# Kernel optimization log

Hardware: AMD Instinct MI355X
Metric: run time of the kernel (lower is better)

Reference implementation:

```python
import jax, jax.numpy as jnp
import numpy as np
import math

D_MODEL = 128
N_HEADS = 4
DIM_FF = 256
B, L = 4, 2048
EPS = 1e-5
NEG = -1e9


def _layernorm(x, g, b):
    mu = jnp.mean(x, axis=-1, keepdims=True)
    var = jnp.mean((x - mu) ** 2, axis=-1, keepdims=True)
    return (x - mu) * jax.lax.rsqrt(var + EPS) * g + b


def setup_inputs() -> dict:
    key = jax.random.key(0)
    ks = jax.random.split(key, 16)
    s = 1.0 / math.sqrt(D_MODEL)
    return {
        "h": jax.random.normal(ks[0], (B, L, D_MODEL), jnp.float32),
        "attn_bias": jax.random.normal(ks[1], (B, N_HEADS, L, L), jnp.float32),
        "node_mask": jax.random.randint(ks[2], (B, L), 0, 2).astype(jnp.float32),
        "sparse_mask": jax.random.randint(ks[3], (B, L, L), 0, 2).astype(bool),
        "w_qkv": jax.random.normal(ks[4], (3 * D_MODEL, D_MODEL), jnp.float32) * s,
        "b_qkv": jnp.zeros((3 * D_MODEL,), jnp.float32),
        "w_out": jax.random.normal(ks[5], (D_MODEL, D_MODEL), jnp.float32) * s,
        "b_out": jnp.zeros((D_MODEL,), jnp.float32),
        "w_ff1": jax.random.normal(ks[6], (DIM_FF, D_MODEL), jnp.float32) * s,
        "b_ff1": jnp.zeros((DIM_FF,), jnp.float32),
        "w_ff2": jax.random.normal(ks[7], (D_MODEL, DIM_FF), jnp.float32) * (1.0 / math.sqrt(DIM_FF)),
        "b_ff2": jnp.zeros((D_MODEL,), jnp.float32),
        "ln1_g": jnp.ones((D_MODEL,), jnp.float32),
        "ln1_b": jnp.zeros((D_MODEL,), jnp.float32),
        "ln2_g": jnp.ones((D_MODEL,), jnp.float32),
        "ln2_b": jnp.zeros((D_MODEL,), jnp.float32),
    }


def reference(h, attn_bias, node_mask, sparse_mask, w_qkv, b_qkv, w_out, b_out,
              w_ff1, b_ff1, w_ff2, b_ff2, ln1_g, ln1_b, ln2_g, ln2_b):
    bsz, lsz, dsz = h.shape
    dk = dsz // N_HEADS
    qkv = h @ w_qkv.T + b_qkv  # [B,L,3D]
    q, k, v = jnp.split(qkv, 3, axis=-1)
    # [B,L,D] -> [B,H,L,dk]
    q = q.reshape(bsz, lsz, N_HEADS, dk).transpose(0, 2, 1, 3)
    k = k.reshape(bsz, lsz, N_HEADS, dk).transpose(0, 2, 1, 3)
    v = v.reshape(bsz, lsz, N_HEADS, dk).transpose(0, 2, 1, 3)
    scores = jnp.einsum("bhqd,bhkd->bhqk", q, k) / math.sqrt(dk)
    scores = scores + attn_bias
    scores = jnp.where(sparse_mask[:, None, :, :], scores, NEG)
    key_mask = node_mask[:, None, None, :] > 0
    scores = jnp.where(key_mask, scores, NEG)
    attn = jax.nn.softmax(scores, axis=-1)
    attn = attn * (node_mask[:, None, :, None] > 0).astype(attn.dtype)
    out = jnp.einsum("bhqk,bhkd->bhqd", attn, v)
    out = out.transpose(0, 2, 1, 3).reshape(bsz, lsz, dsz)
    out = out @ w_out.T + b_out
    h1 = _layernorm(h + out, ln1_g, ln1_b)
    ff = jax.nn.relu(h1 @ w_ff1.T + b_ff1) @ w_ff2.T + b_ff2
    h2 = _layernorm(h1 + ff, ln2_g, ln2_b)
    return h2 * node_mask[:, :, None]
```

## Files before the change

kernel.cpp:

```cpp
#include <hip/hip_runtime.h>
#include <math.h>

#define NEG_INF (-1e9f)
#define EPS 1e-5f

typedef __attribute__((ext_vector_type(8))) short short8;
typedef __attribute__((ext_vector_type(4))) float floatx4;

__device__ __forceinline__ unsigned short f2bf(float x) {
    union { float f; unsigned u; } v; v.f = x;
    unsigned r = v.u + 0x7fffu + ((v.u >> 16) & 1u);
    return (unsigned short)(r >> 16);
}

__device__ __forceinline__ void gl2lds16(const void* g, void* l) {
    __builtin_amdgcn_global_load_lds(
        (const __attribute__((address_space(1))) unsigned int*)g,
        (__attribute__((address_space(3))) unsigned int*)l, 16, 0, 0);
}

__global__ void prep_kernel(const unsigned int* __restrict__ sm, int* __restrict__ flag,
                            const float* __restrict__ nm, unsigned int* __restrict__ nmb) {
    if (blockIdx.x == 0) {
        __shared__ int bad;
        if (threadIdx.x == 0) bad = 0;
        __syncthreads();
        for (int i = threadIdx.x; i < 4096; i += 256) {
            if (sm[i] > 1u) bad = 1;
        }
        __syncthreads();
        if (threadIdx.x == 0) *flag = bad;
    } else {
        const int t = threadIdx.x;
        const int b = t >> 6, w32 = t & 63;
        unsigned u = 0;
#pragma unroll
        for (int j = 0; j < 32; ++j)
            u |= (nm[b * 2048 + w32 * 32 + j] > 0.f ? 1u : 0u) << j;
        nmb[t] = u;
    }
}

__global__ void mask_prep_kernel(const unsigned char* __restrict__ smraw,
                                 const int* __restrict__ flag,
                                 const unsigned int* __restrict__ nmb,
                                 unsigned int* __restrict__ cbits) {
    const int idx = blockIdx.x * 256 + threadIdx.x;
    const int b = idx >> 17;
    const int q = (idx >> 6) & 2047;
    const int w32 = idx & 63;
    unsigned u = 0;
    if (*flag) {
        const uint4* p = reinterpret_cast<const uint4*>(
            smraw + (size_t)(b * 2048 + q) * 2048 + w32 * 32);
        uint4 a = p[0], c = p[1];
        unsigned wd0 = a.x, wd1 = a.y, wd2 = a.z, wd3 = a.w;
        unsigned wd4 = c.x, wd5 = c.y, wd6 = c.z, wd7 = c.w;
#define BYTES4(v, sh) \
        u |= ((v) & 0xffu ? 1u : 0u) << (sh); \
        u |= ((v) & 0xff00u ? 1u : 0u) << ((sh) + 1); \
        u |= ((v) & 0xff0000u ? 1u : 0u) << ((sh) + 2); \
        u |= ((v) & 0xff000000u ? 1u : 0u) << ((sh) + 3);
        BYTES4(wd0, 0) BYTES4(wd1, 4) BYTES4(wd2, 8) BYTES4(wd3, 12)
        BYTES4(wd4, 16) BYTES4(wd5, 20) BYTES4(wd6, 24) BYTES4(wd7, 28)
#undef BYTES4
    } else {
        const uint4* p = reinterpret_cast<const uint4*>(
            reinterpret_cast<const unsigned int*>(smraw) + (size_t)(b * 2048 + q) * 2048 + w32 * 32);
#pragma unroll
        for (int wi = 0; wi < 8; ++wi) {
            uint4 a = p[wi];
            u |= (a.x ? 1u : 0u) << (wi * 4);
            u |= (a.y ? 1u : 0u) << (wi * 4 + 1);
            u |= (a.z ? 1u : 0u) << (wi * 4 + 2);
            u |= (a.w ? 1u : 0u) << (wi * 4 + 3);
        }
    }
    cbits[idx] = u & nmb[b * 64 + w32];
}

__global__ void transpose_all_kernel(const float* __restrict__ w_qkv, const float* __restrict__ w_out,
                                     const float* __restrict__ w_ff1, const float* __restrict__ w_ff2,
                                     float* __restrict__ wqkvT, float* __restrict__ woutT,
                                     float* __restrict__ wff1T, float* __restrict__ wff2T) {
    int idx = blockIdx.x * 256 + threadIdx.x;
    if (idx < 49152) {
        int r = idx / 128, c = idx % 128;
        wqkvT[c * 384 + r] = w_qkv[idx];
    } else if (idx < 65536) {
        int i = idx - 49152; int r = i / 128, c = i % 128;
        woutT[c * 128 + r] = w_out[i];
    } else if (idx < 98304) {
        int i = idx - 65536; int r = i / 128, c = i % 128;
        wff1T[c * 256 + r] = w_ff1[i];
    } else {
        int i = idx - 98304; int r = i / 256, c = i % 256;
        wff2T[c * 128 + r] = w_ff2[i];
    }
}

__global__ void qkv_kernel(const float* __restrict__ h, const float* __restrict__ wT,
                           const float* __restrict__ bqkv,
                           unsigned short* __restrict__ qb, unsigned short* __restrict__ kbm,
                           unsigned short* __restrict__ vtb) {
    __shared__ __align__(16) float hs[16 * 128];
    const int tid = threadIdx.x;
    const int row0 = blockIdx.x * 16;
    for (int i = tid; i < 2048; i += 384) hs[i] = h[row0 * 128 + i];
    __syncthreads();

    const int c = tid;
    float acc[16];
#pragma unroll
    for (int r = 0; r < 16; ++r) acc[r] = 0.f;

    for (int d0 = 0; d0 < 128; d0 += 4) {
        float w0 = wT[(d0 + 0) * 384 + c];
        float w1 = wT[(d0 + 1) * 384 + c];
        float w2 = wT[(d0 + 2) * 384 + c];
        float w3 = wT[(d0 + 3) * 384 + c];
#pragma unroll
        for (int r = 0; r < 16; ++r) {
            float4 h4 = *reinterpret_cast<const float4*>(&hs[r * 128 + d0]);
            acc[r] = fmaf(w0, h4.x, acc[r]);
            acc[r] = fmaf(w1, h4.y, acc[r]);
            acc[r] = fmaf(w2, h4.z, acc[r]);
            acc[r] = fmaf(w3, h4.w, acc[r]);
        }
    }
    const int part = c >> 7;
    const int cc = c & 127;
    const int head = cc >> 5;
    const int dd = cc & 31;
    const float bias = bqkv[c];
    const float scale = (part == 0) ? 0.17677669529663687f : 1.0f;
#pragma unroll
    for (int r = 0; r < 16; ++r) {
        int grow = row0 + r;
        int b = grow >> 11, l = grow & 2047;
        int bh = b * 4 + head;
        unsigned short val = f2bf((acc[r] + bias) * scale);
        if (part == 0)      qb[((size_t)bh * 2048 + l) * 32 + dd] = val;
        else if (part == 1) kbm[((size_t)bh * 2048 + l) * 32 + dd] = val;
        else                vtb[((size_t)bh * 32 + dd) * 2048 + l] = val;
    }
}

__global__ __launch_bounds__(256, 2) void attn_kernel(
        const unsigned short* __restrict__ qb, const unsigned short* __restrict__ kbm,
        const unsigned short* __restrict__ vtb, const float* __restrict__ bias,
        const unsigned int* __restrict__ cbits, const float* __restrict__ nmask,
        float* __restrict__ aout) {
    __shared__ __align__(16) unsigned short k_lds[2][64 * 32];
    __shared__ __align__(16) unsigned short v_lds[2][32 * 64];
    __shared__ __align__(16) float bias_lds[2][64 * 64];
    __shared__ __align__(16) unsigned short p_lds[4][16 * 72];

    const int tid = threadIdx.x;
    const int w = tid >> 6, L = tid & 63;
    const int lb = (blockIdx.x & 7) * 64 + (blockIdx.x >> 3);
    const int bh = lb >> 5, qt = lb & 31;
    const int b = bh >> 2, hh = bh & 3;
    const int q0b = qt * 64;
    const int q = L & 15, g = L >> 4;

    const unsigned short* kb_g = kbm + (size_t)bh * 2048 * 32;
    const unsigned short* vb_g = vtb + (size_t)bh * 32 * 2048;
    const float* bias_q0 = bias + ((size_t)bh * 2048 + q0b) * 2048;
    const short8 qf = *reinterpret_cast<const short8*>(
        qb + ((size_t)bh * 2048 + q0b + w * 16 + q) * 32 + g * 8);
    const unsigned int* crow = cbits + (size_t)(b * 2048 + q0b + w * 16 + q) * 64;

    const int r_k = tid >> 2;
    const size_t k_src0 = (size_t)r_k * 32 + (((tid & 3) ^ (r_k & 3)) << 3);
    const int d_v = tid >> 3;
    const size_t v_src0 = (size_t)d_v * 2048 + (((tid & 7) ^ (d_v & 7)) << 3);
    const int br = tid >> 4;
    const int bsw = ((tid & 15) ^ br) << 2;

    auto stage = [&](int buf, int kt) {
        const int k0 = kt * 64;
        gl2lds16(kb_g + (size_t)k0 * 32 + k_src0, (char*)(&k_lds[buf][0]) + w * 1024);
        gl2lds16(vb_g + k0 + v_src0, (char*)(&v_lds[buf][0]) + w * 1024);
#pragma unroll
        for (int i = 0; i < 4; ++i)
            gl2lds16(bias_q0 + (size_t)(br + 16 * i) * 2048 + k0 + bsw,
                     (char*)(&bias_lds[buf][0]) + i * 4096 + w * 1024);
    };

    stage(0, 0);
    __syncthreads();

    float mrun = -3.0e38f, lrun = 0.f;
    floatx4 o0 = {0.f, 0.f, 0.f, 0.f}, o1 = {0.f, 0.f, 0.f, 0.f};
    const floatx4 zacc = {0.f, 0.f, 0.f, 0.f};
    unsigned short* pl = &p_lds[w][q * 72];

    const int ksw = (g ^ (q & 3)) << 4;
    const int vsw0 = ((g) ^ (q & 7)) << 4;
    const int vsw1 = ((g + 4) ^ (q & 7)) << 4;
    const int brow = (w * 16 + q) * 256;

    for (int t = 0; t < 32; ++t) {
        const int cur = t & 1;
        if (t + 1 < 32) stage(cur ^ 1, t + 1);

        const char* kl = (const char*)(&k_lds[cur][0]);
        short8 kf0 = *reinterpret_cast<const short8*>(kl + (q     ) * 64 + ksw);
        short8 kf1 = *reinterpret_cast<const short8*>(kl + (16 + q) * 64 + ksw);
        short8 kf2 = *reinterpret_cast<const short8*>(kl + (32 + q) * 64 + ksw);
        short8 kf3 = *reinterpret_cast<const short8*>(kl + (48 + q) * 64 + ksw);
        const char* vl = (const char*)(&v_lds[cur][0]);
        short8 vf00 = *reinterpret_cast<const short8*>(vl + (q     ) * 128 + vsw0);
        short8 vf01 = *reinterpret_cast<const short8*>(vl + (q     ) * 128 + vsw1);
        short8 vf10 = *reinterpret_cast<const short8*>(vl + (16 + q) * 128 + vsw0);
        short8 vf11 = *reinterpret_cast<const short8*>(vl + (16 + q) * 128 + vsw1);
        uint2 cw = *reinterpret_cast<const uint2*>(crow + t * 2);

        float s[16];
        {
            floatx4 r0 = __builtin_amdgcn_mfma_f32_16x16x32_bf16(kf0, qf, zacc, 0, 0, 0);
            floatx4 r1 = __builtin_amdgcn_mfma_f32_16x16x32_bf16(kf1, qf, zacc, 0, 0, 0);
            floatx4 r2 = __builtin_amdgcn_mfma_f32_16x16x32_bf16(kf2, qf, zacc, 0, 0, 0);
            floatx4 r3 = __builtin_amdgcn_mfma_f32_16x16x32_bf16(kf3, qf, zacc, 0, 0, 0);
            s[0] = r0[0]; s[1] = r0[1]; s[2] = r0[2]; s[3] = r0[3];
            s[4] = r1[0]; s[5] = r1[1]; s[6] = r1[2]; s[7] = r1[3];
            s[8] = r2[0]; s[9] = r2[1]; s[10] = r2[2]; s[11] = r2[3];
            s[12] = r3[0]; s[13] = r3[1]; s[14] = r3[2]; s[15] = r3[3];
        }
        const char* bl = (const char*)(&bias_lds[cur][0]);
        float4 bq0 = *reinterpret_cast<const float4*>(bl + brow + (((0 + g) ^ q) << 4));
        float4 bq1 = *reinterpret_cast<const float4*>(bl + brow + (((4 + g) ^ q) << 4));
        float4 bq2 = *reinterpret_cast<const float4*>(bl + brow + (((8 + g) ^ q) << 4));
        float4 bq3 = *reinterpret_cast<const float4*>(bl + brow + (((12 + g) ^ q) << 4));
        float bvv[16];
        bvv[0] = bq0.x; bvv[1] = bq0.y; bvv[2] = bq0.z; bvv[3] = bq0.w;
        bvv[4] = bq1.x; bvv[5] = bq1.y; bvv[6] = bq1.z; bvv[7] = bq1.w;
        bvv[8] = bq2.x; bvv[9] = bq2.y; bvv[10] = bq2.z; bvv[11] = bq2.w;
        bvv[12] = bq3.x; bvv[13] = bq3.y; bvv[14] = bq3.z; bvv[15] = bq3.w;
#pragma unroll
        for (int i = 0; i < 16; ++i) {
            const int mm = i >> 2, reg = i & 3;
            const unsigned word = (mm < 2) ? cw.x : cw.y;
            const int sh = 16 * (mm & 1) + 4 * g + reg;
            const bool keep = (word >> sh) & 1;
            s[i] = keep ? (s[i] + bvv[i]) : NEG_INF;
        }
        float tm = s[0];
#pragma unroll
        for (int i = 1; i < 16; ++i) tm = fmaxf(tm, s[i]);
        tm = fmaxf(tm, __shfl_xor(tm, 16));
        tm = fmaxf(tm, __shfl_xor(tm, 32));
        const float mn = fmaxf(mrun, tm);
        const float f = __expf(mrun - mn);
        mrun = mn;
        float p[16], ts = 0.f;
#pragma unroll
        for (int i = 0; i < 16; ++i) { p[i] = __expf(s[i] - mn); ts += p[i]; }
        ts += __shfl_xor(ts, 16);
        ts += __shfl_xor(ts, 32);
        lrun = lrun * f + ts;
        o0 *= f; o1 *= f;
#pragma unroll
        for (int mm = 0; mm < 4; ++mm) {
            unsigned u0 = (unsigned)f2bf(p[4 * mm]) | ((unsigned)f2bf(p[4 * mm + 1]) << 16);
            unsigned u1 = (unsigned)f2bf(p[4 * mm + 2]) | ((unsigned)f2bf(p[4 * mm + 3]) << 16);
            *reinterpret_cast<unsigned int*>(pl + 16 * mm + 4 * g) = u0;
            *reinterpret_cast<unsigned int*>(pl + 16 * mm + 4 * g + 2) = u1;
        }
        short8 pb0 = *reinterpret_cast<const short8*>(pl + g * 8);
        short8 pb1 = *reinterpret_cast<const short8*>(pl + 32 + g * 8);
        o0 = __builtin_amdgcn_mfma_f32_16x16x32_bf16(vf00, pb0, o0, 0, 0, 0);
        o0 = __builtin_amdgcn_mfma_f32_16x16x32_bf16(vf01, pb1, o0, 0, 0, 0);
        o1 = __builtin_amdgcn_mfma_f32_16x16x32_bf16(vf10, pb0, o1, 0, 0, 0);
        o1 = __builtin_amdgcn_mfma_f32_16x16x32_bf16(vf11, pb1, o1, 0, 0, 0);

        __syncthreads();
    }

    const int qrow = q0b + w * 16 + q;
    const float nmq = nmask[b * 2048 + qrow];
    const float inv = (nmq > 0.f) ? (1.f / lrun) : 0.f;
    float* op = aout + ((size_t)b * 2048 + qrow) * 128 + hh * 32 + g * 4;
    *reinterpret_cast<float4*>(op) = make_float4(o0[0] * inv, o0[1] * inv, o0[2] * inv, o0[3] * inv);
    *reinterpret_cast<float4*>(op + 16) = make_float4(o1[0] * inv, o1[1] * inv, o1[2] * inv, o1[3] * inv);
}

__device__ __forceinline__ void ln_stats(const float* buf, float* mu_s, float* rs_s, int tid) {
    int row = tid >> 4, sl = tid & 15;
    float4 x0 = *reinterpret_cast<const float4*>(&buf[row * 128 + sl * 8]);
    float4 x1 = *reinterpret_cast<const float4*>(&buf[row * 128 + sl * 8 + 4]);
    float sum = x0.x + x0.y + x0.z + x0.w + x1.x + x1.y + x1.z + x1.w;
    float sq = x0.x * x0.x + x0.y * x0.y + x0.z * x0.z + x0.w * x0.w +
               x1.x * x1.x + x1.y * x1.y + x1.z * x1.z + x1.w * x1.w;
#pragma unroll
    for (int off = 8; off > 0; off >>= 1) {
        sum += __shfl_xor(sum, off);
        sq += __shfl_xor(sq, off);
    }
    if (sl == 0) {
        float mu = sum * (1.f / 128.f);
        float var = sq * (1.f / 128.f) - mu * mu;
        mu_s[row] = mu;
        rs_s[row] = rsqrtf(var + EPS);
    }
}

__global__ void epilogue_kernel(const float* __restrict__ aout, const float* __restrict__ h,
                                const float* __restrict__ woutT, const float* __restrict__ bout,
                                const float* __restrict__ wff1T, const float* __restrict__ bff1,
                                const float* __restrict__ wff2T, const float* __restrict__ bff2,
                                const float* __restrict__ g1, const float* __restrict__ b1,
                                const float* __restrict__ g2, const float* __restrict__ b2,
                                const float* __restrict__ nmask, float* __restrict__ out) {
    __shared__ __align__(16) float A[16 * 128];
    __shared__ __align__(16) float Hb[16 * 128];
    __shared__ __align__(16) float F[16 * 256];
    __shared__ float mu_s[16], rs_s[16];

    const int tid = threadIdx.x;
    const int row0 = blockIdx.x * 16;
    for (int i = tid; i < 2048; i += 256) {
        A[i] = aout[row0 * 128 + i];
        Hb[i] = h[row0 * 128 + i];
    }
    __syncthreads();

    const int g = tid >> 7, c = tid & 127;

    float acc[8];
#pragma unroll
    for (int r = 0; r < 8; ++r) acc[r] = 0.f;
    for (int d0 = 0; d0 < 128; d0 += 4) {
        float w0 = woutT[(d0 + 0) * 128 + c];
        float w1 = woutT[(d0 + 1) * 128 + c];
        float w2 = woutT[(d0 + 2) * 128 + c];
        float w3 = woutT[(d0 + 3) * 128 + c];
#pragma unroll
        for (int r = 0; r < 8; ++r) {
            float4 a4 = *reinterpret_cast<const float4*>(&A[(g * 8 + r) * 128 + d0]);
            acc[r] = fmaf(w0, a4.x, acc[r]);
            acc[r] = fmaf(w1, a4.y, acc[r]);
            acc[r] = fmaf(w2, a4.z, acc[r]);
            acc[r] = fmaf(w3, a4.w, acc[r]);
        }
    }
    float bo = bout[c];
#pragma unroll
    for (int r = 0; r < 8; ++r) {
        int row = g * 8 + r;
        Hb[row * 128 + c] += acc[r] + bo;
    }
    __syncthreads();

    ln_stats(Hb, mu_s, rs_s, tid);
    __syncthreads();
    float g1c = g1[c], b1c = b1[c];
#pragma unroll
    for (int r = 0; r < 8; ++r) {
        int row = g * 8 + r;
        float v = (Hb[row * 128 + c] - mu_s[row]) * rs_s[row] * g1c + b1c;
        Hb[row * 128 + c] = v;
    }
    __syncthreads();

    {
        const int j = tid;
        float a2[16];
#pragma unroll
        for (int r = 0; r < 16; ++r) a2[r] = 0.f;
        for (int d0 = 0; d0 < 128; d0 += 4) {
            float w0 = wff1T[(d0 + 0) * 256 + j];
            float w1 = wff1T[(d0 + 1) * 256 + j];
            float w2 = wff1T[(d0 + 2) * 256 + j];
            float w3 = wff1T[(d0 + 3) * 256 + j];
#pragma unroll
            for (int r = 0; r < 16; ++r) {
                float4 h4 = *reinterpret_cast<const float4*>(&Hb[r * 128 + d0]);
                a2[r] = fmaf(w0, h4.x, a2[r]);
                a2[r] = fmaf(w1, h4.y, a2[r]);
                a2[r] = fmaf(w2, h4.z, a2[r]);
                a2[r] = fmaf(w3, h4.w, a2[r]);
            }
        }
        float bj = bff1[j];
#pragma unroll
        for (int r = 0; r < 16; ++r) F[r * 256 + j] = fmaxf(a2[r] + bj, 0.f);
    }
    __syncthreads();

    float a3[8];
#pragma unroll
    for (int r = 0; r < 8; ++r) a3[r] = 0.f;
    for (int d0 = 0; d0 < 256; d0 += 4) {
        float w0 = wff2T[(d0 + 0) * 128 + c];
        float w1 = wff2T[(d0 + 1) * 128 + c];
        float w2 = wff2T[(d0 + 2) * 128 + c];
        float w3 = wff2T[(d0 + 3) * 128 + c];
#pragma unroll
        for (int r = 0; r < 8; ++r) {
            float4 f4 = *reinterpret_cast<const float4*>(&F[(g * 8 + r) * 256 + d0]);
            a3[r] = fmaf(w0, f4.x, a3[r]);
            a3[r] = fmaf(w1, f4.y, a3[r]);
            a3[r] = fmaf(w2, f4.z, a3[r]);
            a3[r] = fmaf(w3, f4.w, a3[r]);
        }
    }
    float bo2 = bff2[c];
#pragma unroll
    for (int r = 0; r < 8; ++r) {
        int row = g * 8 + r;
        A[row * 128 + c] = a3[r] + bo2 + Hb[row * 128 + c];
    }
    __syncthreads();

    ln_stats(A, mu_s, rs_s, tid);
    __syncthreads();
    float g2c = g2[c], b2c = b2[c];
#pragma unroll
    for (int r = 0; r < 8; ++r) {
        int row = g * 8 + r;
        float nm = nmask[row0 + row];
        float v = (A[row * 128 + c] - mu_s[row]) * rs_s[row] * g2c + b2c;
        out[(row0 + row) * 128 + c] = v * nm;
    }
}

extern "C" void kernel_launch(void* const* d_in, const int* in_sizes, int n_in,
                              void* d_out, int out_size, void* d_ws, size_t ws_size,
                              hipStream_t stream) {
    const float* h = (const float*)d_in[0];
    const float* bias = (const float*)d_in[1];
    const float* nmask = (const float*)d_in[2];
    const void* smask = d_in[3];
    const float* w_qkv = (const float*)d_in[4];
    const float* b_qkv = (const float*)d_in[5];
    const float* w_out = (const float*)d_in[6];
    const float* b_out = (const float*)d_in[7];
    const float* w_ff1 = (const float*)d_in[8];
    const float* b_ff1 = (const float*)d_in[9];
    const float* w_ff2 = (const float*)d_in[10];
    const float* b_ff2 = (const float*)d_in[11];
    const float* g1 = (const float*)d_in[12];
    const float* b1 = (const float*)d_in[13];
    const float* g2 = (const float*)d_in[14];
    const float* b2 = (const float*)d_in[15];
    float* out = (float*)d_out;

    char* wsb = (char*)d_ws;
    float* aoutw = (float*)wsb;
    unsigned short* qb  = (unsigned short*)(wsb + (4 << 20));
    unsigned short* kbm = (unsigned short*)(wsb + (6 << 20));
    unsigned short* vtb = (unsigned short*)(wsb + (8 << 20));
    unsigned int* cbits = (unsigned int*)(wsb + (10 << 20));
    unsigned int* nmb   = (unsigned int*)(wsb + (12 << 20));
    float* wqkvT = (float*)(wsb + (12 << 20) + 4096);
    float* woutT = wqkvT + 384 * 128;
    float* wff1T = woutT + 128 * 128;
    float* wff2T = wff1T + 256 * 128;
    int* smflag = (int*)(wff2T + 128 * 256);

    prep_kernel<<<2, 256, 0, stream>>>((const unsigned int*)smask, smflag, nmask, nmb);
    mask_prep_kernel<<<2048, 256, 0, stream>>>((const unsigned char*)smask, smflag, nmb, cbits);
    transpose_all_kernel<<<512, 256, 0, stream>>>(w_qkv, w_out, w_ff1, w_ff2,
                                                  wqkvT, woutT, wff1T, wff2T);
    qkv_kernel<<<512, 384, 0, stream>>>(h, wqkvT, b_qkv, qb, kbm, vtb);
    attn_kernel<<<512, 256, 0, stream>>>(qb, kbm, vtb, bias, cbits, nmask, aoutw);
    epilogue_kernel<<<512, 256, 0, stream>>>(aoutw, h, woutT, b_out, wff1T, b_ff1,
                                             wff2T, b_ff2, g1, b1, g2, b2, nmask, out);
}
```

Before: 165.0 us.

## Prefetch two tiles ahead in attention and merge prep with weight transpose

The attention loop now issues K/V/bias tile loads two iterations ahead into the double buffer. It uses explicit vmcnt waits and split barriers instead of a full __syncthreads each step, so more global-to-LDS traffic overlaps the MFMA and softmax work. The weight transpose and the mask/flag prep kernels are merged into one launch to cut a kernel launch. The hand-counted vmcnt(6) depends on exactly six loads per stage, which is fragile if the compiler adds or reorders other memory ops.

```diff
diff --git a/kernel.cpp b/kernel.cpp
--- a/kernel.cpp
+++ b/kernel.cpp
@@ -19,9 +19,28 @@
         (__attribute__((address_space(3))) unsigned int*)l, 16, 0, 0);
 }
 
-__global__ void prep_kernel(const unsigned int* __restrict__ sm, int* __restrict__ flag,
-                            const float* __restrict__ nm, unsigned int* __restrict__ nmb) {
-    if (blockIdx.x == 0) {
+__global__ void transpose_prep_kernel(const float* __restrict__ w_qkv, const float* __restrict__ w_out,
+                                      const float* __restrict__ w_ff1, const float* __restrict__ w_ff2,
+                                      float* __restrict__ wqkvT, float* __restrict__ woutT,
+                                      float* __restrict__ wff1T, float* __restrict__ wff2T,
+                                      const unsigned int* __restrict__ sm, int* __restrict__ flag,
+                                      const float* __restrict__ nm, unsigned int* __restrict__ nmb) {
+    if (blockIdx.x < 512) {
+        int idx = blockIdx.x * 256 + threadIdx.x;
+        if (idx < 49152) {
+            int r = idx / 128, c = idx % 128;
+            wqkvT[c * 384 + r] = w_qkv[idx];
+        } else if (idx < 65536) {
+            int i = idx - 49152; int r = i / 128, c = i % 128;
+            woutT[c * 128 + r] = w_out[i];
+        } else if (idx < 98304) {
+            int i = idx - 65536; int r = i / 128, c = i % 128;
+            wff1T[c * 256 + r] = w_ff1[i];
+        } else {
+            int i = idx - 98304; int r = i / 256, c = i % 256;
+            wff2T[c * 128 + r] = w_ff2[i];
+        }
+    } else if (blockIdx.x == 512) {
         __shared__ int bad;
         if (threadIdx.x == 0) bad = 0;
         __syncthreads();
@@ -79,26 +98,6 @@
     cbits[idx] = u & nmb[b * 64 + w32];
 }
 
-__global__ void transpose_all_kernel(const float* __restrict__ w_qkv, const float* __restrict__ w_out,
-                                     const float* __restrict__ w_ff1, const float* __restrict__ w_ff2,
-                                     float* __restrict__ wqkvT, float* __restrict__ woutT,
-                                     float* __restrict__ wff1T, float* __restrict__ wff2T) {
-    int idx = blockIdx.x * 256 + threadIdx.x;
-    if (idx < 49152) {
-        int r = idx / 128, c = idx % 128;
-        wqkvT[c * 384 + r] = w_qkv[idx];
-    } else if (idx < 65536) {
-        int i = idx - 49152; int r = i / 128, c = i % 128;
-        woutT[c * 128 + r] = w_out[i];
-    } else if (idx < 98304) {
-        int i = idx - 65536; int r = i / 128, c = i % 128;
-        wff1T[c * 256 + r] = w_ff1[i];
-    } else {
-        int i = idx - 98304; int r = i / 256, c = i % 256;
-        wff2T[c * 128 + r] = w_ff2[i];
-    }
-}
-
 __global__ void qkv_kernel(const float* __restrict__ h, const float* __restrict__ wT,
                            const float* __restrict__ bqkv,
                            unsigned short* __restrict__ qb, unsigned short* __restrict__ kbm,
@@ -189,7 +188,9 @@
     };
 
     stage(0, 0);
-    __syncthreads();
+    stage(1, 1);
+    asm volatile("s_waitcnt vmcnt(6)" ::: "memory");
+    __builtin_amdgcn_s_barrier();
 
     float mrun = -3.0e38f, lrun = 0.f;
     floatx4 o0 = {0.f, 0.f, 0.f, 0.f}, o1 = {0.f, 0.f, 0.f, 0.f};
@@ -203,7 +204,6 @@
 
     for (int t = 0; t < 32; ++t) {
         const int cur = t & 1;
-        if (t + 1 < 32) stage(cur ^ 1, t + 1);
 
         const char* kl = (const char*)(&k_lds[cur][0]);
         short8 kf0 = *reinterpret_cast<const short8*>(kl + (q     ) * 64 + ksw);
@@ -275,7 +275,16 @@
         o1 = __builtin_amdgcn_mfma_f32_16x16x32_bf16(vf10, pb0, o1, 0, 0, 0);
         o1 = __builtin_amdgcn_mfma_f32_16x16x32_bf16(vf11, pb1, o1, 0, 0, 0);
 
-        __syncthreads();
+        if (t < 31) {
+            __builtin_amdgcn_s_barrier();
+            if (t + 2 < 32) {
+                stage(cur, t + 2);
+                asm volatile("s_waitcnt vmcnt(6)" ::: "memory");
+            } else {
+                asm volatile("s_waitcnt vmcnt(0)" ::: "memory");
+            }
+            __builtin_amdgcn_s_barrier();
+        }
     }
 
     const int qrow = q0b + w * 16 + q;
@@ -460,10 +469,11 @@
     float* wff2T = wff1T + 256 * 128;
     int* smflag = (int*)(wff2T + 128 * 256);
 
-    prep_kernel<<<2, 256, 0, stream>>>((const unsigned int*)smask, smflag, nmask, nmb);
+    transpose_prep_kernel<<<514, 256, 0, stream>>>(w_qkv, w_out, w_ff1, w_ff2,
+                                                   wqkvT, woutT, wff1T, wff2T,
+                                                   (const unsigned int*)smask, smflag,
+                                                   nmask, nmb);
     mask_prep_kernel<<<2048, 256, 0, stream>>>((const unsigned char*)smask, smflag, nmb, cbits);
-    transpose_all_kernel<<<512, 256, 0, stream>>>(w_qkv, w_out, w_ff1, w_ff2,
-                                                  wqkvT, woutT, wff1T, wff2T);
     qkv_kernel<<<512, 384, 0, stream>>>(h, wqkvT, b_qkv, qb, kbm, vtb);
     attn_kernel<<<512, 256, 0, stream>>>(qb, kbm, vtb, bias, cbits, nmask, aoutw);
     epilogue_kernel<<<512, 256, 0, stream>>>(aoutw, h, woutT, b_out, wff1T, b_ff1,
```

Result: faster. 157.6 us (median of 2 runs) (-4.5%).
